# Kernel optimization log

Measured on AMD Instinct MI355X. Metric: run time of the kernel, lower is better.

## Reference

```python
import jax, jax.numpy as jnp
import numpy as np

PATCH = 16; NBINS = 8; ITERS = 20; REG = 0.1; EPS = 1e-6

M1 = jnp.array([[0.4122214708, 0.5363325363, 0.0514459929],
                [0.2119034982, 0.6806995451, 0.1073969566],
                [0.0883024619, 0.2817188376, 0.6299787005]], dtype=jnp.float32)
M2 = jnp.array([[0.2104542553, 0.793617785, -0.0040720468],
                [1.9779984951, -2.428592205, 0.4505937099],
                [0.0259040371, 0.7827717662, -0.808675766]], dtype=jnp.float32)


def srgb_to_oklab(x):
    x = jnp.clip(x, 0.0, 1.0)
    lin = jnp.where(x <= 0.04045, x / 12.92,
                    jnp.maximum((x + 0.055) / 1.055, 0.0) ** 2.4)
    px = jnp.moveaxis(lin, 1, -1)                       # (B,H,W,3)
    lms = jnp.maximum(px @ M1.T, 0.0)
    lms_g = jnp.sign(lms) * jnp.maximum(jnp.abs(lms), 1e-12) ** (1.0 / 3.0)
    lab = lms_g @ M2.T
    return jnp.moveaxis(lab, -1, 1)                     # (B,3,H,W)


def extract_histograms(oklab):
    B, _, H, W = oklab.shape
    ps, nb = PATCH, NBINS
    Ph, Pw = H // ps, W // ps                           # H,W divisible by ps -> no reflect pad
    p = oklab.reshape(B, 3, Ph, ps, Pw, ps)
    patches = jnp.transpose(p, (0, 2, 4, 3, 5, 1)).reshape(B * Ph * Pw, ps * ps, 3)
    lo = patches.min(axis=(0, 1)) - 0.01
    hi = patches.max(axis=(0, 1)) + 0.01
    narrow = (hi - lo) < 1e-4
    lo = jnp.where(narrow, lo - 0.05, lo)
    hi = jnp.where(narrow, hi + 0.05, hi)
    # midpoints of linspace(lo, hi, nb+1) edges
    t = (jnp.arange(nb, dtype=oklab.dtype) + 0.5) / nb
    centers = lo[:, None] + (hi - lo)[:, None] * t[None, :]          # (3,nb)
    grid = jnp.stack(jnp.meshgrid(centers[0], centers[1], centers[2],
                                  indexing='ij'), axis=-1).reshape(-1, 3)  # (N,3)
    # squared distance has the same argmin as euclidean cdist
    d2 = (jnp.sum(patches ** 2, -1, keepdims=True)
          - 2.0 * (patches @ grid.T)
          + jnp.sum(grid ** 2, -1)[None, None, :])      # (P, ps*ps, N)
    assign = jnp.argmin(d2, axis=-1)                    # (P, ps*ps)
    P, N = patches.shape[0], nb ** 3
    hist = jnp.zeros((P, N), oklab.dtype).at[jnp.arange(P)[:, None], assign].add(1.0)
    return hist, grid


def sinkhorn_emd(hist_r, hist_t, grid):
    sum_r = hist_r.sum(-1, keepdims=True)
    sum_t = hist_t.sum(-1, keepdims=True)
    empty = (sum_r[:, 0] <= EPS) | (sum_t[:, 0] <= EPS)
    hr = hist_r / jnp.maximum(sum_r, EPS)
    ht = hist_t / jnp.maximum(sum_t, EPS)
    d2 = jnp.sum((grid[:, None, :] - grid[None, :, :]) ** 2, -1)     # (N,N)
    cost = jnp.where(d2 > 0, jnp.sqrt(jnp.where(d2 > 0, d2, 1.0)), 0.0)  # safe cdist
    K = jnp.exp(-cost / REG)

    def body(carry, _):
        u, _v = carry
        v = ht / (u @ K.T + EPS)
        u = hr / (v @ K + EPS)
        return (u, v), None

    u0 = jnp.ones_like(hr)
    (u, v), _ = jax.lax.scan(body, (u0, u0), None, length=ITERS)
    # sum_ij u_i K_ij c_ij v_j  (avoids materializing the (P,N,N) transport plan)
    emd = jnp.einsum('pi,ij,pj->p', u, K * cost, v)
    emd = jnp.nan_to_num(emd, nan=0.0, posinf=0.0, neginf=0.0)
    return jnp.where(empty, 0.0, emd)


def forward(ref, tgt):
    B, _, H, W = ref.shape
    Ph, Pw = H // PATCH, W // PATCH
    hist_r, grid_r = extract_histograms(srgb_to_oklab(ref))
    hist_t, grid_t = extract_histograms(srgb_to_oklab(tgt))
    grid = (grid_r + grid_t) / 2.0
    emd = sinkhorn_emd(hist_r, hist_t, grid)
    emd_map = emd.reshape(B, 1, Ph, Pw)
    # half-pixel bilinear == F.interpolate(mode='bilinear', align_corners=False)
    return jax.image.resize(emd_map, (B, 1, H, W), method='bilinear')


def setup_inputs() -> dict:
    key = jax.random.key(0)
    k1, k2 = jax.random.split(key)
    ref = jax.random.uniform(k1, (4, 3, 256, 256), dtype=jnp.float32)
    tgt = jax.random.uniform(k2, (4, 3, 256, 256), dtype=jnp.float32)
    return {"ref": ref, "tgt": tgt}


def reference(ref, tgt):
    return forward(ref, tgt)
```

## Files before the change

### kernel.cpp

```cpp
#include <hip/hip_runtime.h>
#include <hip/hip_bf16.h>


#define LAB_STRIDE 786432
#define SP 520

typedef __attribute__((ext_vector_type(8))) _Float16 half8_t;
typedef __attribute__((ext_vector_type(4))) _Float16 half4_t;
typedef __attribute__((ext_vector_type(4))) float floatx4;

__device__ __forceinline__ float hw_exp2(float x) { return __builtin_amdgcn_exp2f(x); }
__device__ __forceinline__ float hw_log2(float x) { return __builtin_amdgcn_logf(x); }

__device__ __forceinline__ unsigned enc_f(float f) {
    unsigned u = __float_as_uint(f);
    return (u & 0x80000000u) ? ~u : (u | 0x80000000u);
}
__device__ __forceinline__ float dec_f(unsigned k) {
    unsigned u = (k & 0x80000000u) ? (k ^ 0x80000000u) : ~k;
    return __uint_as_float(u);
}

__device__ __forceinline__ float s2lin(float x) {
    x = fminf(fmaxf(x, 0.f), 1.f);
    return (x <= 0.04045f) ? (x * (1.f / 12.92f))
                           : hw_exp2(2.4f * hw_log2((x + 0.055f) * (1.f / 1.055f)));
}
__device__ __forceinline__ float cbrt_fast(float l) {
    return hw_exp2(0.33333333333f * hw_log2(fmaxf(l, 1e-12f)));
}

__device__ __forceinline__ void compute_lohi(
        const float* __restrict__ bmn, const float* __restrict__ bmx,
        int img, float lo[3], float hi[3]) {
    int lane = threadIdx.x & 63;
    for (int c = 0; c < 3; ++c) {
        float mn = 3.4e38f, mx = -3.4e38f;
        for (int i = lane; i < 128; i += 64) {
            mn = fminf(mn, bmn[(img * 128 + i) * 3 + c]);
            mx = fmaxf(mx, bmx[(img * 128 + i) * 3 + c]);
        }
        for (int s = 1; s < 64; s <<= 1) {
            mn = fminf(mn, __shfl_xor(mn, s));
            mx = fmaxf(mx, __shfl_xor(mx, s));
        }
        float l = mn - 0.01f, h = mx + 0.01f;
        if (h - l < 1e-4f) { l -= 0.05f; h += 0.05f; }
        lo[c] = l; hi[c] = h;
    }
}

__global__ __launch_bounds__(256) void oklab_minmax_kernel(
        const float* __restrict__ ref, const float* __restrict__ tgt,
        float* __restrict__ lab, float* __restrict__ bmn, float* __restrict__ bmx) {
    int blk = blockIdx.x, tid = threadIdx.x;
    int img = blk >> 7;
    const float* src = img ? tgt : ref;
    float* dst = lab + img * LAB_STRIDE;

    __shared__ unsigned smin[3], smax[3];
    if (tid < 3) { smin[tid] = 0xFFFFFFFFu; smax[tid] = 0u; }
    __syncthreads();

    float fmn[3] = {3.4e38f, 3.4e38f, 3.4e38f};
    float fmx[3] = {-3.4e38f, -3.4e38f, -3.4e38f};
    int base = (blk & 127) * 2048;
    #pragma unroll
    for (int k = 0; k < 8; ++k) {
        int px = base + k * 256 + tid;
        int bi = px >> 16, rem = px & 65535;
        float r = s2lin(src[(bi * 3 + 0) * 65536 + rem]);
        float g = s2lin(src[(bi * 3 + 1) * 65536 + rem]);
        float b = s2lin(src[(bi * 3 + 2) * 65536 + rem]);
        float l0 = fmaxf(0.4122214708f * r + 0.5363325363f * g + 0.0514459929f * b, 0.f);
        float l1 = fmaxf(0.2119034982f * r + 0.6806995451f * g + 0.1073969566f * b, 0.f);
        float l2 = fmaxf(0.0883024619f * r + 0.2817188376f * g + 0.6299787005f * b, 0.f);
        float g0 = (l0 > 0.f) ? cbrt_fast(l0) : 0.f;
        float g1 = (l1 > 0.f) ? cbrt_fast(l1) : 0.f;
        float g2 = (l2 > 0.f) ? cbrt_fast(l2) : 0.f;
        float L  = 0.2104542553f * g0 + 0.793617785f  * g1 - 0.0040720468f * g2;
        float A  = 1.9779984951f * g0 - 2.428592205f  * g1 + 0.4505937099f * g2;
        float Bv = 0.0259040371f * g0 + 0.7827717662f * g1 - 0.808675766f  * g2;
        dst[(bi * 3 + 0) * 65536 + rem] = L;
        dst[(bi * 3 + 1) * 65536 + rem] = A;
        dst[(bi * 3 + 2) * 65536 + rem] = Bv;
        fmn[0] = fminf(fmn[0], L);  fmx[0] = fmaxf(fmx[0], L);
        fmn[1] = fminf(fmn[1], A);  fmx[1] = fmaxf(fmx[1], A);
        fmn[2] = fminf(fmn[2], Bv); fmx[2] = fmaxf(fmx[2], Bv);
    }
    for (int s = 1; s < 64; s <<= 1) {
        for (int c = 0; c < 3; ++c) {
            fmn[c] = fminf(fmn[c], __shfl_xor(fmn[c], s));
            fmx[c] = fmaxf(fmx[c], __shfl_xor(fmx[c], s));
        }
    }
    if ((tid & 63) == 0) {
        for (int c = 0; c < 3; ++c) {
            atomicMin(&smin[c], enc_f(fmn[c]));
            atomicMax(&smax[c], enc_f(fmx[c]));
        }
    }
    __syncthreads();
    if (tid < 3) {
        bmn[blk * 3 + tid] = dec_f(smin[tid]);
        bmx[blk * 3 + tid] = dec_f(smax[tid]);
    }
}

__global__ __launch_bounds__(256) void pack_hist_kernel(
        const float* __restrict__ lab,
        const float* __restrict__ bmn, const float* __restrict__ bmx,
        float* __restrict__ hr, float* __restrict__ ht,
        _Float16* __restrict__ kmf, _Float16* __restrict__ kcf) {
    int blk = blockIdx.x, tid = threadIdx.x;
    float lo0[3], hi0[3], lo1[3], hi1[3];
    compute_lohi(bmn, bmx, 0, lo0, hi0);
    compute_lohi(bmn, bmx, 1, lo1, hi1);

    if (blk < 256) {
        float cen[3][8];
        for (int c = 0; c < 3; ++c)
            for (int k = 0; k < 8; ++k) {
                float t = (k + 0.5f) * 0.125f;
                cen[c][k] = 0.5f * ((lo0[c] + (hi0[c] - lo0[c]) * t)
                                  + (lo1[c] + (hi1[c] - lo1[c]) * t));
            }
        int g = blk * 256 + tid;
        int half = g & 1, lane = (g >> 1) & 63, kc = (g >> 7) & 15, jt = g >> 11;
        int n = jt * 16 + (lane & 15);
        int kb = kc * 32 + ((lane >> 4) << 3) + half * 4;
        float n0 = cen[0][n >> 6], n1 = cen[1][(n >> 3) & 7], n2 = cen[2][n & 7];
        half4_t vm, vc;
        #pragma unroll
        for (int r = 0; r < 4; ++r) {
            int k = kb + r;
            float d0 = cen[0][k >> 6] - n0;
            float d1 = cen[1][(k >> 3) & 7] - n1;
            float d2 = cen[2][k & 7] - n2;
            float dd = d0 * d0 + d1 * d1 + d2 * d2;
            float cost = (dd > 0.f) ? __fsqrt_rn(dd) : 0.f;
            float kv = hw_exp2(-cost * 14.426950408889634f);
            vm[r] = (_Float16)kv;
            vc[r] = (_Float16)(kv * cost);
        }
        int base = ((kc * 32 + jt) * 64 + lane) * 8 + half * 4;
        *(half4_t*)(kmf + base) = vm;
        *(half4_t*)(kcf + base) = vc;
    }

    int img = blk >> 10;
    int p = blk & 1023;
    float cenI[3][8];
    {
        const float* lo = img ? lo1 : lo0;
        const float* hi = img ? hi1 : hi0;
        for (int c = 0; c < 3; ++c)
            for (int k = 0; k < 8; ++k)
                cenI[c][k] = lo[c] + (hi[c] - lo[c]) * ((k + 0.5f) * 0.125f);
    }
    __shared__ unsigned hcnt[512];
    hcnt[tid] = 0u; hcnt[tid + 256] = 0u;
    __syncthreads();
    int b = p >> 8, ph = (p >> 4) & 15, pw = p & 15;
    int y = tid >> 4, x = tid & 15;
    int rem = (ph * 16 + y) * 256 + (pw * 16 + x);
    const float* lb = lab + img * LAB_STRIDE;
    int kidx[3];
    for (int c = 0; c < 3; ++c) {
        float vv = lb[(b * 3 + c) * 65536 + rem];
        int best = 0; float bd = 3.4e38f;
        for (int k = 0; k < 8; ++k) {
            float d = vv - cenI[c][k];
            float ds = d * d;
            if (ds < bd) { bd = ds; best = k; }
        }
        kidx[c] = best;
    }
    atomicAdd(&hcnt[kidx[0] * 64 + kidx[1] * 8 + kidx[2]], 1u);
    __syncthreads();
    float* dst = img ? ht : hr;
    dst[p * 512 + tid]       = (float)hcnt[tid]       * (1.f / 256.f);
    dst[p * 512 + tid + 256] = (float)hcnt[tid + 256] * (1.f / 256.f);
}

__global__ __launch_bounds__(512, 2) void sinkhorn_kernel(
        const float* __restrict__ hr, const float* __restrict__ ht,
        const _Float16* __restrict__ kmf, const _Float16* __restrict__ kcf,
        float* __restrict__ emd) {
    __shared__ __align__(16) _Float16 U[8 * SP], V[8 * SP];
    __shared__ __align__(16) _Float16 hrs[4096], hts[4096];
    __shared__ __align__(16) _Float16 Kc3[49152];
    __shared__ float ebuf[8];
    int tid = threadIdx.x;
    int wave = tid >> 6, lane = tid & 63;
    int pbase = blockIdx.x * 8;

    for (int i = tid; i < 4096; i += 512) {
        hrs[i] = (_Float16)hr[pbase * 512 + i];
        hts[i] = (_Float16)ht[pbase * 512 + i];
    }
    for (int i = tid; i < 8 * SP; i += 512) U[i] = (_Float16)1.0f;
    for (int i = tid; i < 6144; i += 512)
        *(half8_t*)(Kc3 + i * 8) = *(const half8_t*)(kmf + i * 8);
    if (tid < 8) ebuf[tid] = 0.f;
    __syncthreads();

    int mrow = lane & 15;
    int kgrp = (lane >> 4) << 3;
    int jt0 = wave * 4;
    int rq = lane >> 4;
    int colc = lane & 15;

    for (int h = 0; h < 40; ++h) {
        const _Float16* S = (h & 1) ? V : U;
        _Float16* D = (h & 1) ? U : V;
        const _Float16* hs = (h & 1) ? hrs : hts;
        floatx4 acc[4] = {{0,0,0,0},{0,0,0,0},{0,0,0,0},{0,0,0,0}};
        #pragma unroll
        for (int kc = 0; kc < 3; ++kc) {
            half8_t a = *(const half8_t*)&S[mrow * SP + kc * 32 + kgrp];
            #pragma unroll
            for (int q = 0; q < 4; ++q) {
                half8_t b = *(const half8_t*)&Kc3[((kc * 32 + jt0 + q) * 64 + lane) * 8];
                acc[q] = __builtin_amdgcn_mfma_f32_16x16x32_f16(a, b, acc[q], 0, 0, 0);
            }
        }
        #pragma unroll
        for (int kc = 3; kc < 16; ++kc) {
            half8_t a = *(const half8_t*)&S[mrow * SP + kc * 32 + kgrp];
            const _Float16* bb = kmf + ((kc * 32 + jt0) * 64 + lane) * 8;
            #pragma unroll
            for (int q = 0; q < 4; ++q) {
                half8_t b = *(const half8_t*)(bb + q * 512);
                acc[q] = __builtin_amdgcn_mfma_f32_16x16x32_f16(a, b, acc[q], 0, 0, 0);
            }
        }
        if (rq < 2) {
            #pragma unroll
            for (int q = 0; q < 4; ++q) {
                int col = (jt0 + q) * 16 + colc;
                #pragma unroll
                for (int r = 0; r < 4; ++r) {
                    int row = rq * 4 + r;
                    float d = (float)hs[row * 512 + col] / (acc[q][r] + 1e-6f);
                    D[row * SP + col] = (_Float16)fminf(d, 60000.f);
                }
            }
        }
        __syncthreads();
    }

    {
        floatx4 acc[4] = {{0,0,0,0},{0,0,0,0},{0,0,0,0},{0,0,0,0}};
        #pragma unroll
        for (int kc = 0; kc < 16; ++kc) {
            half8_t a = *(const half8_t*)&U[mrow * SP + kc * 32 + kgrp];
            const _Float16* bb = kcf + ((kc * 32 + jt0) * 64 + lane) * 8;
            #pragma unroll
            for (int q = 0; q < 4; ++q) {
                half8_t b = *(const half8_t*)(bb + q * 512);
                acc[q] = __builtin_amdgcn_mfma_f32_16x16x32_f16(a, b, acc[q], 0, 0, 0);
            }
        }
        float pe[4] = {0.f, 0.f, 0.f, 0.f};
        if (rq < 2) {
            #pragma unroll
            for (int q = 0; q < 4; ++q) {
                int col = (jt0 + q) * 16 + colc;
                #pragma unroll
                for (int r = 0; r < 4; ++r)
                    pe[r] += acc[q][r] * (float)V[(rq * 4 + r) * SP + col];
            }
        }
        for (int s = 1; s < 16; s <<= 1) {
            #pragma unroll
            for (int r = 0; r < 4; ++r) pe[r] += __shfl_xor(pe[r], s);
        }
        if (colc == 0 && rq < 2) {
            #pragma unroll
            for (int r = 0; r < 4; ++r)
                atomicAdd(&ebuf[rq * 4 + r], pe[r]);
        }
        __syncthreads();
        if (tid < 8) {
            float e = ebuf[tid];
            emd[pbase + tid] = __builtin_isfinite(e) ? e : 0.f;
        }
    }
}

__global__ __launch_bounds__(256) void upsample_kernel(
        const float* __restrict__ emd, float* __restrict__ out) {
    #pragma unroll
    for (int k = 0; k < 4; ++k) {
        int idx = blockIdx.x * 1024 + k * 256 + threadIdx.x;
        int b = idx >> 16;
        int rem = idx & 65535;
        int y = rem >> 8, x = rem & 255;
        float sy = (y + 0.5f) * 0.0625f - 0.5f;
        float sx = (x + 0.5f) * 0.0625f - 0.5f;
        float fy0 = floorf(sy), fx0 = floorf(sx);
        float fy = sy - fy0, fx = sx - fx0;
        int y0 = (int)fy0, x0 = (int)fx0;
        int y0c = min(max(y0, 0), 15), y1c = min(max(y0 + 1, 0), 15);
        int x0c = min(max(x0, 0), 15), x1c = min(max(x0 + 1, 0), 15);
        const float* e = emd + b * 256;
        float v00 = e[y0c * 16 + x0c], v01 = e[y0c * 16 + x1c];
        float v10 = e[y1c * 16 + x0c], v11 = e[y1c * 16 + x1c];
        out[idx] = (1.f - fy) * ((1.f - fx) * v00 + fx * v01)
                 + fy * ((1.f - fx) * v10 + fx * v11);
    }
}

extern "C" void kernel_launch(void* const* d_in, const int* in_sizes, int n_in,
                              void* d_out, int out_size, void* d_ws, size_t ws_size,
                              hipStream_t stream) {
    const float* ref = (const float*)d_in[0];
    const float* tgt = (const float*)d_in[1];
    float* out = (float*)d_out;

    float* lab = (float*)d_ws;
    float* bmn = lab + 2 * LAB_STRIDE;
    float* bmx = bmn + 768;
    float* hr  = bmx + 768;
    float* ht  = hr + 524288;
    float* emd = ht + 524288;
    _Float16* kmf = (_Float16*)(emd + 1024);
    _Float16* kcf = kmf + 262144;

    oklab_minmax_kernel<<<256, 256, 0, stream>>>(ref, tgt, lab, bmn, bmx);
    pack_hist_kernel<<<2048, 256, 0, stream>>>(lab, bmn, bmx, hr, ht, kmf, kcf);
    sinkhorn_kernel<<<128, 512, 0, stream>>>(hr, ht, kmf, kcf, emd);
    upsample_kernel<<<256, 256, 0, stream>>>(emd, out);
}
```

Baseline: 220.2 us.

## Fuse histogram binning into Sinkhorn kernel and cache more of K in LDS

Moves per-patch histogram construction out of the pack kernel and into the Sinkhorn kernel. Each block bins its own 8 patches for both images using LDS atomics and keeps the histogram values in registers, so the hr/ht global round trip and their LDS copies go away. The freed LDS lets the kernel cache 4 of the 16 K chunks instead of 3. Binning now uses a direct floor-based index instead of a nearest-center search, which can differ from argmin exactly at bin boundaries. Removing the (512,2) occupancy hint and enlarging LDS may lower occupancy, and the 8 sequential binning rounds add serial work at the start of each block.

```diff
diff --git a/kernel.cpp b/kernel.cpp
--- a/kernel.cpp
+++ b/kernel.cpp
@@ -107,103 +107,54 @@
     }
 }
 
-__global__ __launch_bounds__(256) void pack_hist_kernel(
-        const float* __restrict__ lab,
+__global__ __launch_bounds__(256) void pack_k_kernel(
         const float* __restrict__ bmn, const float* __restrict__ bmx,
-        float* __restrict__ hr, float* __restrict__ ht,
         _Float16* __restrict__ kmf, _Float16* __restrict__ kcf) {
     int blk = blockIdx.x, tid = threadIdx.x;
     float lo0[3], hi0[3], lo1[3], hi1[3];
     compute_lohi(bmn, bmx, 0, lo0, hi0);
     compute_lohi(bmn, bmx, 1, lo1, hi1);
-
-    if (blk < 256) {
-        float cen[3][8];
-        for (int c = 0; c < 3; ++c)
-            for (int k = 0; k < 8; ++k) {
-                float t = (k + 0.5f) * 0.125f;
-                cen[c][k] = 0.5f * ((lo0[c] + (hi0[c] - lo0[c]) * t)
-                                  + (lo1[c] + (hi1[c] - lo1[c]) * t));
-            }
-        int g = blk * 256 + tid;
-        int half = g & 1, lane = (g >> 1) & 63, kc = (g >> 7) & 15, jt = g >> 11;
-        int n = jt * 16 + (lane & 15);
-        int kb = kc * 32 + ((lane >> 4) << 3) + half * 4;
-        float n0 = cen[0][n >> 6], n1 = cen[1][(n >> 3) & 7], n2 = cen[2][n & 7];
-        half4_t vm, vc;
-        #pragma unroll
-        for (int r = 0; r < 4; ++r) {
-            int k = kb + r;
-            float d0 = cen[0][k >> 6] - n0;
-            float d1 = cen[1][(k >> 3) & 7] - n1;
-            float d2 = cen[2][k & 7] - n2;
-            float dd = d0 * d0 + d1 * d1 + d2 * d2;
-            float cost = (dd > 0.f) ? __fsqrt_rn(dd) : 0.f;
-            float kv = hw_exp2(-cost * 14.426950408889634f);
-            vm[r] = (_Float16)kv;
-            vc[r] = (_Float16)(kv * cost);
-        }
-        int base = ((kc * 32 + jt) * 64 + lane) * 8 + half * 4;
-        *(half4_t*)(kmf + base) = vm;
-        *(half4_t*)(kcf + base) = vc;
-    }
-
-    int img = blk >> 10;
-    int p = blk & 1023;
-    float cenI[3][8];
-    {
-        const float* lo = img ? lo1 : lo0;
-        const float* hi = img ? hi1 : hi0;
-        for (int c = 0; c < 3; ++c)
-            for (int k = 0; k < 8; ++k)
-                cenI[c][k] = lo[c] + (hi[c] - lo[c]) * ((k + 0.5f) * 0.125f);
-    }
-    __shared__ unsigned hcnt[512];
-    hcnt[tid] = 0u; hcnt[tid + 256] = 0u;
-    __syncthreads();
-    int b = p >> 8, ph = (p >> 4) & 15, pw = p & 15;
-    int y = tid >> 4, x = tid & 15;
-    int rem = (ph * 16 + y) * 256 + (pw * 16 + x);
-    const float* lb = lab + img * LAB_STRIDE;
-    int kidx[3];
-    for (int c = 0; c < 3; ++c) {
-        float vv = lb[(b * 3 + c) * 65536 + rem];
-        int best = 0; float bd = 3.4e38f;
+    float cen[3][8];
+    for (int c = 0; c < 3; ++c)
         for (int k = 0; k < 8; ++k) {
-            float d = vv - cenI[c][k];
-            float ds = d * d;
-            if (ds < bd) { bd = ds; best = k; }
-        }
-        kidx[c] = best;
-    }
-    atomicAdd(&hcnt[kidx[0] * 64 + kidx[1] * 8 + kidx[2]], 1u);
-    __syncthreads();
-    float* dst = img ? ht : hr;
-    dst[p * 512 + tid]       = (float)hcnt[tid]       * (1.f / 256.f);
-    dst[p * 512 + tid + 256] = (float)hcnt[tid + 256] * (1.f / 256.f);
-}
-
-__global__ __launch_bounds__(512, 2) void sinkhorn_kernel(
-        const float* __restrict__ hr, const float* __restrict__ ht,
+            float t = (k + 0.5f) * 0.125f;
+            cen[c][k] = 0.5f * ((lo0[c] + (hi0[c] - lo0[c]) * t)
+                              + (lo1[c] + (hi1[c] - lo1[c]) * t));
+        }
+    int g = blk * 256 + tid;
+    int half = g & 1, lane = (g >> 1) & 63, kc = (g >> 7) & 15, jt = g >> 11;
+    int n = jt * 16 + (lane & 15);
+    int kb = kc * 32 + ((lane >> 4) << 3) + half * 4;
+    float n0 = cen[0][n >> 6], n1 = cen[1][(n >> 3) & 7], n2 = cen[2][n & 7];
+    half4_t vm, vc;
+    #pragma unroll
+    for (int r = 0; r < 4; ++r) {
+        int k = kb + r;
+        float d0 = cen[0][k >> 6] - n0;
+        float d1 = cen[1][(k >> 3) & 7] - n1;
+        float d2 = cen[2][k & 7] - n2;
+        float dd = d0 * d0 + d1 * d1 + d2 * d2;
+        float cost = (dd > 0.f) ? __fsqrt_rn(dd) : 0.f;
+        float kv = hw_exp2(-cost * 14.426950408889634f);
+        vm[r] = (_Float16)kv;
+        vc[r] = (_Float16)(kv * cost);
+    }
+    int base = ((kc * 32 + jt) * 64 + lane) * 8 + half * 4;
+    *(half4_t*)(kmf + base) = vm;
+    *(half4_t*)(kcf + base) = vc;
+}
+
+__global__ __launch_bounds__(512) void sinkhorn_kernel(
+        const float* __restrict__ lab,
+        const float* __restrict__ bmn, const float* __restrict__ bmx,
         const _Float16* __restrict__ kmf, const _Float16* __restrict__ kcf,
         float* __restrict__ emd) {
     __shared__ __align__(16) _Float16 U[8 * SP], V[8 * SP];
-    __shared__ __align__(16) _Float16 hrs[4096], hts[4096];
-    __shared__ __align__(16) _Float16 Kc3[49152];
+    __shared__ __align__(16) _Float16 Kc4[65536];
     __shared__ float ebuf[8];
     int tid = threadIdx.x;
     int wave = tid >> 6, lane = tid & 63;
     int pbase = blockIdx.x * 8;
-
-    for (int i = tid; i < 4096; i += 512) {
-        hrs[i] = (_Float16)hr[pbase * 512 + i];
-        hts[i] = (_Float16)ht[pbase * 512 + i];
-    }
-    for (int i = tid; i < 8 * SP; i += 512) U[i] = (_Float16)1.0f;
-    for (int i = tid; i < 6144; i += 512)
-        *(half8_t*)(Kc3 + i * 8) = *(const half8_t*)(kmf + i * 8);
-    if (tid < 8) ebuf[tid] = 0.f;
-    __syncthreads();
 
     int mrow = lane & 15;
     int kgrp = (lane >> 4) << 3;
@@ -211,22 +162,81 @@
     int rq = lane >> 4;
     int colc = lane & 15;
 
+    float lo_[2][3], inv_[2][3];
+    {
+        float lo0[3], hi0[3], lo1[3], hi1[3];
+        compute_lohi(bmn, bmx, 0, lo0, hi0);
+        compute_lohi(bmn, bmx, 1, lo1, hi1);
+        for (int c = 0; c < 3; ++c) {
+            lo_[0][c] = lo0[c]; inv_[0][c] = 8.f / (hi0[c] - lo0[c]);
+            lo_[1][c] = lo1[c]; inv_[1][c] = 8.f / (hi1[c] - lo1[c]);
+        }
+    }
+
+    float hreg[2][4][4];
+    unsigned* scr = (unsigned*)Kc4;
+    for (int s = 0; s < 8; ++s) {
+        scr[tid] = 0u; scr[tid + 512] = 0u;
+        __syncthreads();
+        int grp = tid >> 8;
+        int pair = s * 2 + grp;
+        int img = pair >> 3, pl = pair & 7;
+        int p = pbase + pl;
+        int b = p >> 8, ph = (p >> 4) & 15, pw = p & 15;
+        int px = tid & 255;
+        int y = px >> 4, x = px & 15;
+        int rem = (ph * 16 + y) * 256 + pw * 16 + x;
+        const float* lb = lab + img * LAB_STRIDE + b * 3 * 65536 + rem;
+        int bin = 0;
+        #pragma unroll
+        for (int c = 0; c < 3; ++c) {
+            float v = lb[c * 65536];
+            int k = (int)floorf((v - lo_[img][c]) * inv_[img][c]);
+            k = min(max(k, 0), 7);
+            bin = bin * 8 + k;
+        }
+        atomicAdd(&scr[grp * 512 + bin], 1u);
+        __syncthreads();
+        #pragma unroll
+        for (int g2 = 0; g2 < 2; ++g2) {
+            int pr2 = s * 2 + g2;
+            int im2 = pr2 >> 3, pl2 = pr2 & 7;
+            if (rq < 2 && (pl2 >> 2) == rq) {
+                int r = pl2 & 3;
+                #pragma unroll
+                for (int q = 0; q < 4; ++q)
+                    hreg[im2][q][r] = (float)scr[g2 * 512 + (jt0 + q) * 16 + colc]
+                                    * (1.f / 256.f);
+            }
+        }
+        __syncthreads();
+    }
+    if (rq >= 2)
+        for (int i2 = 0; i2 < 2; ++i2)
+            for (int q = 0; q < 4; ++q)
+                for (int r = 0; r < 4; ++r) hreg[i2][q][r] = 0.f;
+
+    for (int i = tid; i < 8 * SP; i += 512) U[i] = (_Float16)1.0f;
+    for (int i = tid; i < 16384; i += 512)
+        *(half8_t*)(Kc4 + i * 8) = *(const half8_t*)(kmf + i * 8);
+    if (tid < 8) ebuf[tid] = 0.f;
+    __syncthreads();
+
     for (int h = 0; h < 40; ++h) {
         const _Float16* S = (h & 1) ? V : U;
         _Float16* D = (h & 1) ? U : V;
-        const _Float16* hs = (h & 1) ? hrs : hts;
         floatx4 acc[4] = {{0,0,0,0},{0,0,0,0},{0,0,0,0},{0,0,0,0}};
         #pragma unroll
-        for (int kc = 0; kc < 3; ++kc) {
+        for (int kc = 0; kc < 4; ++kc) {
             half8_t a = *(const half8_t*)&S[mrow * SP + kc * 32 + kgrp];
             #pragma unroll
             for (int q = 0; q < 4; ++q) {
-                half8_t b = *(const half8_t*)&Kc3[((kc * 32 + jt0 + q) * 64 + lane) * 8];
+                half8_t b = *(const half8_t*)&Kc4[((kc * 32 + jt0 + q) * 64 + lane) * 8];
                 acc[q] = __builtin_amdgcn_mfma_f32_16x16x32_f16(a, b, acc[q], 0, 0, 0);
             }
         }
         #pragma unroll
-        for (int kc = 3; kc < 16; ++kc) {
+        for (int kc = 4; kc < 16; ++kc) {
             half8_t a = *(const half8_t*)&S[mrow * SP + kc * 32 + kgrp];
             const _Float16* bb = kmf + ((kc * 32 + jt0) * 64 + lane) * 8;
             #pragma unroll
@@ -236,13 +246,14 @@
             }
         }
         if (rq < 2) {
+            const int hi_sel = (h & 1) ? 0 : 1;
             #pragma unroll
             for (int q = 0; q < 4; ++q) {
                 int col = (jt0 + q) * 16 + colc;
                 #pragma unroll
                 for (int r = 0; r < 4; ++r) {
                     int row = rq * 4 + r;
-                    float d = (float)hs[row * 512 + col] / (acc[q][r] + 1e-6f);
+                    float d = hreg[hi_sel][q][r] / (acc[q][r] + 1e-6f);
                     D[row * SP + col] = (_Float16)fminf(d, 60000.f);
                 }
             }
@@ -322,14 +333,12 @@
     float* lab = (float*)d_ws;
     float* bmn = lab + 2 * LAB_STRIDE;
     float* bmx = bmn + 768;
-    float* hr  = bmx + 768;
-    float* ht  = hr + 524288;
-    float* emd = ht + 524288;
+    float* emd = bmx + 768;
     _Float16* kmf = (_Float16*)(emd + 1024);
     _Float16* kcf = kmf + 262144;
 
     oklab_minmax_kernel<<<256, 256, 0, stream>>>(ref, tgt, lab, bmn, bmx);
-    pack_hist_kernel<<<2048, 256, 0, stream>>>(lab, bmn, bmx, hr, ht, kmf, kcf);
-    sinkhorn_kernel<<<128, 512, 0, stream>>>(hr, ht, kmf, kcf, emd);
+    pack_k_kernel<<<256, 256, 0, stream>>>(bmn, bmx, kmf, kcf);
+    sinkhorn_kernel<<<128, 512, 0, stream>>>(lab, bmn, bmx, kmf, kcf, emd);
     upsample_kernel<<<256, 256, 0, stream>>>(emd, out);
 }
```

Result: no change. 215.9 us (-1.9%).
